# Performance work log

Measured on AMD Instinct MI355X. Metric: run time of the kernel, lower is better.

## Reference

```python
import jax, jax.numpy as jnp
import numpy as np

T, N, C, RADIUS = 64, 16, 256, 64
D_OUT = 2 * RADIUS + 1
TAU = 2.0
DECAY = float(np.exp(-1.0 / TAU))  # first-order leaky (LIF) filter decay
WEIGHT0 = 6.53543197272069


def setup_inputs() -> dict:
    key = jax.random.key(0)
    k1, k2 = jax.random.split(key)
    inp = jax.random.uniform(k1, (T, N, C, 2), dtype=jnp.float32)
    delay_param = jnp.arange(-RADIUS, RADIUS + 1, dtype=jnp.float32)[:, None]  # (D_out, 1)
    weight = jnp.asarray(WEIGHT0, dtype=jnp.float32)
    u = jax.random.uniform(k2, (N, C, D_OUT, 2), dtype=jnp.float32)  # bernoulli uniforms
    return {"input": inp, "delay_param": delay_param, "weight": weight, "u": u}


def reference(input, delay_param, weight, u):
    Tn, Nn, Cn, _ = input.shape
    # delay = relu(cat([_delay, -_delay], dim=1))  -> (D_out, 2), nonnegative
    delay = jax.nn.relu(jnp.concatenate([delay_param, -delay_param], axis=1))
    Do = delay.shape[0]
    # input.unsqueeze(-2).repeat(..., D_out, 1) -> (T, N, C, D_out, 2)
    x = jnp.broadcast_to(input[:, :, :, None, :], (Tn, Nn, Cn, Do, 2))
    # stochastic rounding of per-synapse delay
    bd = jnp.broadcast_to(delay[None, None], (Nn, Cn, Do, 2))
    df = jnp.floor(bd)
    rounded = jnp.where(u < bd - df, df + 1.0, df)
    # clamp so the (one-hot) spike at argmax(t) stays inside the window
    spike_t = jnp.argmax(x, axis=0)  # (N, C, D_out, 2)
    rounded = jnp.minimum(rounded, (Tn - 1 - spike_t).astype(rounded.dtype))
    d = rounded.astype(jnp.int32)
    # circular shift along time: out[t] = x[(t - d) % T]
    t_idx = jnp.arange(Tn)[:, None, None, None, None]
    idx = (t_idx - d[None]) % Tn
    shifted = jnp.take_along_axis(x, idx, axis=0)  # (T, N, C, D_out, 2)
    # LIF filter (leaky integrator over time, state reset at t=0)
    def step(v, xt):
        v = v * DECAY + xt
        return v, v
    _, filt = jax.lax.scan(step, jnp.zeros_like(shifted[0]), shifted)
    # scale by fixed synaptic weight and sum over the 2 input channels
    return jnp.sum(filt * weight, axis=-1)  # (T, N, C, D_out)
```

## Files before the change

kernel.cpp:

```cpp
#include <hip/hip_runtime.h>
#include <hip/hip_bf16.h>

#define T_DIM 64
#define NP 4096
#define D_OUTC 129

typedef float v4f __attribute__((ext_vector_type(4)));

__global__ __launch_bounds__(256, 8) void jeffress_kernel(
    const float* __restrict__ input,
    const float* __restrict__ delay_param,
    const float* __restrict__ weight,
    const float* __restrict__ u,
    float* __restrict__ out)
{
    __shared__ float x_lds[2][64];
    __shared__ __hip_bfloat16 G[2][64 * 64];
    __shared__ int shifts[D_OUTC];
    __shared__ int cap[2];

    const int p   = blockIdx.x;
    const int tid = threadIdx.x;
    const int lane = tid & 63, wave = tid >> 6;
    const float DECAY = 0.6065306597126334f;

    if (tid < 128) {
        int ch = wave, t = lane;
        float xv = input[(t * NP + p) * 2 + ch];
        x_lds[ch][t] = xv;
        unsigned b = __float_as_uint(xv);
        b ^= (b & 0x80000000u) ? 0xffffffffu : 0x80000000u;
        unsigned long long key = ((unsigned long long)b << 32) | (unsigned)(63 - t);
        #pragma unroll
        for (int mm = 1; mm < 64; mm <<= 1) {
            unsigned long long o = __shfl_xor(key, mm, 64);
            if (o > key) key = o;
        }
        if (lane == 0) cap[ch] = (int)(key & 0xffffffffull);
    }
    __syncthreads();

    if (tid < 128) {
        int ch = wave, s = lane;
        const float* xs = x_lds[ch];
        __hip_bfloat16* g = G[ch];
        float v = 0.0f;
        #pragma unroll 4
        for (int t = 0; t < 64; ++t) {
            v = v * DECAY + xs[(t - s) & 63];
            g[t * 64 + s] = __float2bfloat16(v);
        }
    } else {
        int c0 = cap[0], c1 = cap[1];
        for (int d = tid - 128; d < D_OUTC; d += 128) {
            float dp = delay_param[d];
            float b0 = fmaxf(dp, 0.0f), b1 = fmaxf(-dp, 0.0f);
            float2 uu = ((const float2*)u)[p * D_OUTC + d];
            float f0 = floorf(b0), f1 = floorf(b1);
            float r0 = (uu.x < b0 - f0) ? f0 + 1.0f : f0;
            float r1 = (uu.y < b1 - f1) ? f1 + 1.0f : f1;
            int s0 = (int)fminf(r0, (float)c0);
            int s1 = (int)fminf(r1, (float)c1);
            shifts[d] = s0 | (s1 << 16);
        }
    }
    __syncthreads();

    const float w = weight[0];
    const int a = (4 - (p & 3)) & 3;
    const int m = (D_OUTC - a) >> 2;
    const int e = D_OUTC - 4 * m;
    const bool isBody  = lane < m;
    const bool isExtra = (lane >= m) && (lane - m < e);

    int o00=0,o01=0,o10=0,o11=0,o20=0,o21=0,o30=0,o31=0;
    int dE = 0;
    if (isBody) {
        int dd = a + 4 * lane;
        int p0 = shifts[dd], p1 = shifts[dd+1], p2 = shifts[dd+2], p3 = shifts[dd+3];
        o00 = (p0 & 0xffff) * 2; o01 = (p0 >> 16) * 2;
        o10 = (p1 & 0xffff) * 2; o11 = (p1 >> 16) * 2;
        o20 = (p2 & 0xffff) * 2; o21 = (p2 >> 16) * 2;
        o30 = (p3 & 0xffff) * 2; o31 = (p3 >> 16) * 2;
    } else if (isExtra) {
        int j = lane - m;
        dE = (j < a) ? j : 4 * m + j;
        int pe = shifts[dE];
        o00 = (pe & 0xffff) * 2; o01 = (pe >> 16) * 2;
    }

    const char* G0b = (const char*)&G[0][0];
    const char* G1b = (const char*)&G[1][0];
    for (int t = wave; t < T_DIM; t += 4) {
        const char* r0 = G0b + t * 128;
        const char* r1 = G1b + t * 128;
        float* rowp = out + (size_t)(t * NP + p) * D_OUTC;
        if (isBody) {
            v4f v;
            v.x = w * (__bfloat162float(*(const __hip_bfloat16*)(r0 + o00)) +
                       __bfloat162float(*(const __hip_bfloat16*)(r1 + o01)));
            v.y = w * (__bfloat162float(*(const __hip_bfloat16*)(r0 + o10)) +
                       __bfloat162float(*(const __hip_bfloat16*)(r1 + o11)));
            v.z = w * (__bfloat162float(*(const __hip_bfloat16*)(r0 + o20)) +
                       __bfloat162float(*(const __hip_bfloat16*)(r1 + o21)));
            v.w = w * (__bfloat162float(*(const __hip_bfloat16*)(r0 + o30)) +
                       __bfloat162float(*(const __hip_bfloat16*)(r1 + o31)));
            *reinterpret_cast<v4f*>(rowp + a + 4 * lane) = v;
        }
        if (isExtra) {
            float vE = w * (__bfloat162float(*(const __hip_bfloat16*)(r0 + o00)) +
                            __bfloat162float(*(const __hip_bfloat16*)(r1 + o01)));
            rowp[dE] = vE;
        }
    }
}

extern "C" void kernel_launch(void* const* d_in, const int* in_sizes, int n_in,
                              void* d_out, int out_size, void* d_ws, size_t ws_size,
                              hipStream_t stream) {
    const float* input       = (const float*)d_in[0];
    const float* delay_param = (const float*)d_in[1];
    const float* weight      = (const float*)d_in[2];
    const float* u           = (const float*)d_in[3];
    float* out = (float*)d_out;

    jeffress_kernel<<<NP, 256, 0, stream>>>(input, delay_param, weight, u, out);
}
```

Baseline: 165.4 us.

## Exploit zero-shift channel to halve LDS gathers and swizzle block order

Since delay is relu of ±delay_param, at most one channel has a nonzero shift per output, so the shift table now encodes which channel is shifted. The unshifted channel's value is read once per row as a broadcast (h0/h1), so each output needs one gathered LDS read instead of two, with a wave-uniform fallback to two reads when both shifts are nonzero (possible only through the clamp). Block indices are also permuted so that consecutive blocks map to positions spread across the problem, which changes the order of global reads and writes. Adds more integer decode work and per-lane selects.

```diff
diff --git a/kernel.cpp b/kernel.cpp
--- a/kernel.cpp
+++ b/kernel.cpp
@@ -6,6 +6,10 @@
 #define D_OUTC 129
 
 typedef float v4f __attribute__((ext_vector_type(4)));
+
+static __device__ __forceinline__ float bfld(const char* p) {
+    return __bfloat162float(*(const __hip_bfloat16*)p);
+}
 
 __global__ __launch_bounds__(256, 8) void jeffress_kernel(
     const float* __restrict__ input,
@@ -19,7 +23,7 @@
     __shared__ int shifts[D_OUTC];
     __shared__ int cap[2];
 
-    const int p   = blockIdx.x;
+    const int p   = ((blockIdx.x & 7) << 9) | (blockIdx.x >> 3);
     const int tid = threadIdx.x;
     const int lane = tid & 63, wave = tid >> 6;
     const float DECAY = 0.6065306597126334f;
@@ -61,7 +65,11 @@
             float r1 = (uu.y < b1 - f1) ? f1 + 1.0f : f1;
             int s0 = (int)fminf(r0, (float)c0);
             int s1 = (int)fminf(r1, (float)c1);
-            shifts[d] = s0 | (s1 << 16);
+            int entry;
+            if (s0 == 0)      entry = s1 | (1 << 6);
+            else if (s1 == 0) entry = s0;
+            else              entry = s0 | (1 << 7) | (s1 << 8);
+            shifts[d] = entry;
         }
     }
     __syncthreads();
@@ -73,44 +81,53 @@
     const bool isBody  = lane < m;
     const bool isExtra = (lane >= m) && (lane - m < e);
 
-    int o00=0,o01=0,o10=0,o11=0,o20=0,o21=0,o30=0,o31=0;
+    int o0=0,o1=0,o2=0,o3=0;
+    int u0=0,u1=0,u2=0,u3=0;
+    int q0=0,q1=0,q2=0,q3=0;
+    int a20=0,a21=0,a22=0,a23=0;
     int dE = 0;
     if (isBody) {
         int dd = a + 4 * lane;
-        int p0 = shifts[dd], p1 = shifts[dd+1], p2 = shifts[dd+2], p3 = shifts[dd+3];
-        o00 = (p0 & 0xffff) * 2; o01 = (p0 >> 16) * 2;
-        o10 = (p1 & 0xffff) * 2; o11 = (p1 >> 16) * 2;
-        o20 = (p2 & 0xffff) * 2; o21 = (p2 >> 16) * 2;
-        o30 = (p3 & 0xffff) * 2; o31 = (p3 >> 16) * 2;
+        int e0 = shifts[dd], e1 = shifts[dd+1], e2 = shifts[dd+2], e3 = shifts[dd+3];
+        o0 = ((e0 >> 6) & 1) * 8192 + (e0 & 63) * 2; u0 = (e0 >> 6) & 1; q0 = (e0 >> 7) & 1; a20 = 8192 + ((e0 >> 8) & 63) * 2;
+        o1 = ((e1 >> 6) & 1) * 8192 + (e1 & 63) * 2; u1 = (e1 >> 6) & 1; q1 = (e1 >> 7) & 1; a21 = 8192 + ((e1 >> 8) & 63) * 2;
+        o2 = ((e2 >> 6) & 1) * 8192 + (e2 & 63) * 2; u2 = (e2 >> 6) & 1; q2 = (e2 >> 7) & 1; a22 = 8192 + ((e2 >> 8) & 63) * 2;
+        o3 = ((e3 >> 6) & 1) * 8192 + (e3 & 63) * 2; u3 = (e3 >> 6) & 1; q3 = (e3 >> 7) & 1; a23 = 8192 + ((e3 >> 8) & 63) * 2;
     } else if (isExtra) {
         int j = lane - m;
         dE = (j < a) ? j : 4 * m + j;
-        int pe = shifts[dE];
-        o00 = (pe & 0xffff) * 2; o01 = (pe >> 16) * 2;
+        int ee = shifts[dE];
+        o0 = ((ee >> 6) & 1) * 8192 + (ee & 63) * 2; u0 = (ee >> 6) & 1; q0 = (ee >> 7) & 1; a20 = 8192 + ((ee >> 8) & 63) * 2;
     }
+    const bool anyboth = __ballot((isBody | isExtra) ? (q0 | q1 | q2 | q3) : 0) != 0ull;
 
-    const char* G0b = (const char*)&G[0][0];
-    const char* G1b = (const char*)&G[1][0];
+    const char* Gb = (const char*)&G[0][0];
     for (int t = wave; t < T_DIM; t += 4) {
-        const char* r0 = G0b + t * 128;
-        const char* r1 = G1b + t * 128;
+        const char* bt = Gb + t * 128;
+        float h0 = bfld(bt);
+        float h1 = bfld(bt + 8192);
         float* rowp = out + (size_t)(t * NP + p) * D_OUTC;
         if (isBody) {
-            v4f v;
-            v.x = w * (__bfloat162float(*(const __hip_bfloat16*)(r0 + o00)) +
-                       __bfloat162float(*(const __hip_bfloat16*)(r1 + o01)));
-            v.y = w * (__bfloat162float(*(const __hip_bfloat16*)(r0 + o10)) +
-                       __bfloat162float(*(const __hip_bfloat16*)(r1 + o11)));
-            v.z = w * (__bfloat162float(*(const __hip_bfloat16*)(r0 + o20)) +
-                       __bfloat162float(*(const __hip_bfloat16*)(r1 + o21)));
-            v.w = w * (__bfloat162float(*(const __hip_bfloat16*)(r0 + o30)) +
-                       __bfloat162float(*(const __hip_bfloat16*)(r1 + o31)));
+            float g0v = bfld(bt + o0), g1v = bfld(bt + o1);
+            float g2v = bfld(bt + o2), g3v = bfld(bt + o3);
+            float v0 = g0v + (u0 ? h0 : h1);
+            float v1 = g1v + (u1 ? h0 : h1);
+            float v2 = g2v + (u2 ? h0 : h1);
+            float v3 = g3v + (u3 ? h0 : h1);
+            if (anyboth) {
+                if (q0) v0 = g0v + bfld(bt + a20);
+                if (q1) v1 = g1v + bfld(bt + a21);
+                if (q2) v2 = g2v + bfld(bt + a22);
+                if (q3) v3 = g3v + bfld(bt + a23);
+            }
+            v4f v; v.x = w * v0; v.y = w * v1; v.z = w * v2; v.w = w * v3;
             *reinterpret_cast<v4f*>(rowp + a + 4 * lane) = v;
         }
         if (isExtra) {
-            float vE = w * (__bfloat162float(*(const __hip_bfloat16*)(r0 + o00)) +
-                            __bfloat162float(*(const __hip_bfloat16*)(r1 + o01)));
-            rowp[dE] = vE;
+            float gv = bfld(bt + o0);
+            float vE = gv + (u0 ? h0 : h1);
+            if (anyboth && q0) vE = gv + bfld(bt + a20);
+            rowp[dE] = w * vE;
         }
     }
 }
```

Result: faster. 157.3 us (-4.9%).
